# Kernel optimization log

Measured on AMD Instinct MI355X. Metric: run time of the kernel, lower is better.

Reference implementation:

```python
import jax, jax.numpy as jnp
import numpy as np

N_NODES = 100000
N_EDGES = 1600000
IN_DIM = 128
OUT_DIM = 128


def setup_inputs() -> dict:
    key = jax.random.key(0)
    k1, k2, k3, k4 = jax.random.split(key, 4)
    x = jax.random.normal(k1, (N_NODES, IN_DIM), dtype=jnp.float32)
    edge_index = jax.random.randint(k2, (2, N_EDGES), 0, N_NODES, dtype=jnp.int64)
    # glorot-ish linear weight, bias, and PReLU per-channel slope (torch default 0.25)
    W = jax.random.normal(k3, (IN_DIM, OUT_DIM), dtype=jnp.float32) * (1.0 / np.sqrt(IN_DIM))
    b = jax.random.normal(k4, (OUT_DIM,), dtype=jnp.float32) * 0.01
    alpha = jnp.full((OUT_DIM,), 0.25, dtype=jnp.float32)
    return {"x": x, "edge_index": edge_index, "W": W, "b": b, "alpha": alpha}


def reference(x, edge_index, W, b, alpha):
    N = x.shape[0]
    # add self loops (GCNConv default add_self_loops=True)
    loop = jnp.arange(N, dtype=edge_index.dtype)
    src = jnp.concatenate([edge_index[0], loop])  # [E+N]
    dst = jnp.concatenate([edge_index[1], loop])
    # symmetric normalization: deg computed at targets (includes self loops)
    ones = jnp.ones(dst.shape[0], dtype=x.dtype)
    deg = jax.ops.segment_sum(ones, dst, num_segments=N)  # [N]
    dinv = jnp.where(deg > 0, jax.lax.rsqrt(deg), 0.0)
    norm = dinv[src] * dinv[dst]  # [E+N]
    # dense linear transform, then gather-normalize-scatter aggregation
    h = x @ W  # [N, OUT_DIM]
    msg = h[src] * norm[:, None]  # [E+N, OUT_DIM]
    agg = jax.ops.segment_sum(msg, dst, num_segments=N) + b  # [N, OUT_DIM]
    # PReLU with per-channel slope
    z = jnp.where(agg > 0, agg, alpha * agg)
    return z
```

## Files before the change

kernel.cpp:

```cpp
#include <hip/hip_runtime.h>
#include <hip/hip_bf16.h>
#include <cstdint>

#define DIM 128
#define BK_SHIFT 7
#define BK_NODES 128
#define MAX_BUCKETS 1024
#define CUR_STRIDE 16
#define ST 4096
#define EPT 16
#define CAP 2560

typedef float f32x4  __attribute__((ext_vector_type(4)));
typedef short bf16x8 __attribute__((ext_vector_type(8)));

__device__ __forceinline__ unsigned bf16_rne(float f) {
    unsigned u = __float_as_uint(f);
    return (u + 0x7fffu + ((u >> 16) & 1u)) >> 16;
}

__global__ __launch_bounds__(256) void init_kernel(const float* __restrict__ x,
                                                   ushort* __restrict__ y,
                                                   const float* __restrict__ W,
                                                   ushort* __restrict__ Wt,
                                                   int* __restrict__ bcursor,
                                                   int N, int pb, int wb, int nbk) {
    int b = blockIdx.x, tid = threadIdx.x;
    if (b < pb) {
        int t = b * 256 + tid;
        if (t < N * (DIM / 4)) {
            float4 v = ((const float4*)x)[t];
            uint2 o;
            o.x = bf16_rne(v.x) | (bf16_rne(v.y) << 16);
            o.y = bf16_rne(v.z) | (bf16_rne(v.w) << 16);
            ((uint2*)y)[t] = o;
        }
    } else if (b < pb + wb) {
        int idx = (b - pb) * 256 + tid;
        if (idx < DIM * DIM) {
            int k = idx >> 7, c = idx & (DIM - 1);
            Wt[c * DIM + k] = (ushort)bf16_rne(W[idx]);
        }
    } else {
        int idx = (b - pb - wb) * 256 + tid;
        if (idx < nbk * CUR_STRIDE) bcursor[idx] = 0;
    }
}

__global__ __launch_bounds__(256) void scatter_kernel(const int* __restrict__ src,
                                                      const int* __restrict__ dst,
                                                      int* __restrict__ bcursor,
                                                      int* __restrict__ bbuf,
                                                      int E, int nbk) {
    __shared__ int h[MAX_BUCKETS];
    for (int i = threadIdx.x; i < nbk; i += 256) h[i] = 0;
    __syncthreads();
    int base = blockIdx.x * ST;
    int bk[EPT], rk[EPT], pk[EPT];
    #pragma unroll
    for (int k = 0; k < EPT; ++k) {
        int e = base + k * 256 + threadIdx.x;
        bk[k] = -1;
        if (e < E) {
            int d = dst[e];
            int b = ((unsigned)d) >> BK_SHIFT;
            bk[k] = b;
            pk[k] = (src[e] << BK_SHIFT) | (d & (BK_NODES - 1));
            rk[k] = atomicAdd(&h[b], 1);
        }
    }
    __syncthreads();
    for (int i = threadIdx.x; i < nbk; i += 256) {
        int c = h[i];
        h[i] = c ? atomicAdd(&bcursor[i * CUR_STRIDE], c) : 0;
    }
    __syncthreads();
    #pragma unroll
    for (int k = 0; k < EPT; ++k) {
        if (bk[k] >= 0) {
            int pos = h[bk[k]] + rk[k];
            if (pos < CAP) bbuf[(size_t)bk[k] * CAP + pos] = pk[k];
        }
    }
}

__global__ __launch_bounds__(256) void build_csr_kernel(const int* __restrict__ bbuf,
                                                        const int* __restrict__ bcursor,
                                                        int* __restrict__ obeg,
                                                        int* __restrict__ oend,
                                                        float* __restrict__ dinv,
                                                        int* __restrict__ csr_src,
                                                        int N) {
    __shared__ int cnt[BK_NODES];
    __shared__ int sc[BK_NODES];
    __shared__ int cur[BK_NODES];
    int b = blockIdx.x, tid = threadIdx.x;
    int count = bcursor[b * CUR_STRIDE];
    if (count > CAP) count = CAP;
    int base = b * CAP;
    if (tid < BK_NODES) cnt[tid] = 0;
    __syncthreads();
    for (int j = tid; j < count; j += 256)
        atomicAdd(&cnt[bbuf[base + j] & (BK_NODES - 1)], 1);
    __syncthreads();
    if (tid < BK_NODES) sc[tid] = cnt[tid];
    __syncthreads();
    for (int d = 1; d < BK_NODES; d <<= 1) {
        int v = (tid >= d && tid < BK_NODES) ? sc[tid - d] : 0;
        __syncthreads();
        if (tid < BK_NODES) sc[tid] += v;
        __syncthreads();
    }
    if (tid < BK_NODES) {
        int node = b * BK_NODES + tid;
        int start = base + sc[tid] - cnt[tid];
        cur[tid] = start;
        if (node < N) {
            obeg[node] = start;
            oend[node] = start + cnt[tid];
            dinv[node] = rsqrtf((float)(cnt[tid] + 1));
        }
    }
    __syncthreads();
    for (int j = tid; j < count; j += 256) {
        int p = bbuf[base + j];
        int pos = atomicAdd(&cur[p & (BK_NODES - 1)], 1);
        csr_src[pos] = p >> BK_SHIFT;
    }
}

__device__ __forceinline__ void agg_accum(float* a, uint4 v, float wt) {
    a[0] += wt * __uint_as_float(v.x << 16);
    a[1] += wt * __uint_as_float(v.x & 0xffff0000u);
    a[2] += wt * __uint_as_float(v.y << 16);
    a[3] += wt * __uint_as_float(v.y & 0xffff0000u);
    a[4] += wt * __uint_as_float(v.z << 16);
    a[5] += wt * __uint_as_float(v.z & 0xffff0000u);
    a[6] += wt * __uint_as_float(v.w << 16);
    a[7] += wt * __uint_as_float(v.w & 0xffff0000u);
}

__global__ __launch_bounds__(256) void agg_kernel(const ushort* __restrict__ y,
                                                  const int* __restrict__ csr_src,
                                                  const int* __restrict__ obeg,
                                                  const int* __restrict__ oend,
                                                  const float* __restrict__ dinv,
                                                  ushort* __restrict__ h, int N) {
    int lane = threadIdx.x & 63;
    int wid  = __builtin_amdgcn_readfirstlane((int)(threadIdx.x >> 6));
    int node = blockIdx.x * 4 + wid;
    if (node >= N) return;
    int g = lane >> 4;
    int m = lane & 15;
    int beg = obeg[node];
    int cnt = oend[node] - beg;
    float di = dinv[node];
    float a[8];
    #pragma unroll
    for (int c = 0; c < 8; ++c) a[c] = 0.f;

    {
        uint4 v = ((const uint4*)(y + (size_t)node * DIM))[m];
        agg_accum(a, v, (g == 0) ? di : 0.f);
    }

    int t = g;
    int nit = (cnt + 7) >> 3;
    for (int it = 0; it < nit; ++it, t += 8) {
        int tB = t + 4;
        int iA = beg + (t  < cnt ? t  : cnt - 1);
        int iB = beg + (tB < cnt ? tB : cnt - 1);
        int sA = csr_src[iA];
        int sB = csr_src[iB];
        float wA = (t  < cnt) ? dinv[sA] : 0.f;
        float wB = (tB < cnt) ? dinv[sB] : 0.f;
        uint4 vA = ((const uint4*)(y + (size_t)sA * DIM))[m];
        uint4 vB = ((const uint4*)(y + (size_t)sB * DIM))[m];
        agg_accum(a, vA, wA);
        agg_accum(a, vB, wB);
    }

    #pragma unroll
    for (int c = 0; c < 8; ++c) {
        a[c] += __shfl_xor(a[c], 16);
        a[c] += __shfl_xor(a[c], 32);
    }

    if (g == 0) {
        uint4 o;
        o.x = bf16_rne(di * a[0]) | (bf16_rne(di * a[1]) << 16);
        o.y = bf16_rne(di * a[2]) | (bf16_rne(di * a[3]) << 16);
        o.z = bf16_rne(di * a[4]) | (bf16_rne(di * a[5]) << 16);
        o.w = bf16_rne(di * a[6]) | (bf16_rne(di * a[7]) << 16);
        ((uint4*)(h + (size_t)node * DIM))[m] = o;
    }
}

__global__ __launch_bounds__(256) void gemm_kernel(const ushort* __restrict__ h,
                                                   const ushort* __restrict__ Wt,
                                                   const float* __restrict__ bias,
                                                   const float* __restrict__ alpha,
                                                   float* __restrict__ out, int N) {
    int lane = threadIdx.x & 63;
    int wv   = threadIdx.x >> 6;
    int rowbase = (blockIdx.x * 4 + wv) * 16;
    int r = lane & 15, quad = lane >> 4;
    f32x4 acc[8];
    #pragma unroll
    for (int ct = 0; ct < 8; ++ct) acc[ct] = (f32x4){0.f, 0.f, 0.f, 0.f};
    int arow = rowbase + r;
    if (arow >= N) arow = N - 1;
    const ushort* ap = h + (size_t)arow * DIM + quad * 8;
    #pragma unroll
    for (int ks = 0; ks < 4; ++ks) {
        bf16x8 a = *(const bf16x8*)(ap + ks * 32);
        #pragma unroll
        for (int ct = 0; ct < 8; ++ct) {
            bf16x8 b = *(const bf16x8*)(Wt + (size_t)(ct * 16 + r) * DIM + ks * 32 + quad * 8);
            acc[ct] = __builtin_amdgcn_mfma_f32_16x16x32_bf16(a, b, acc[ct], 0, 0, 0);
        }
    }
    #pragma unroll
    for (int ct = 0; ct < 8; ++ct) {
        int col = ct * 16 + r;
        float bb = bias[col], al = alpha[col];
        #pragma unroll
        for (int reg = 0; reg < 4; ++reg) {
            int grow = rowbase + quad * 4 + reg;
            if (grow < N) {
                float vv = acc[ct][reg] + bb;
                vv = vv > 0.f ? vv : al * vv;
                out[(size_t)grow * DIM + col] = vv;
            }
        }
    }
}

extern "C" void kernel_launch(void* const* d_in, const int* in_sizes, int n_in,
                              void* d_out, int out_size, void* d_ws, size_t ws_size,
                              hipStream_t stream) {
    const float* x     = (const float*)d_in[0];
    const int*   ei    = (const int*)d_in[1];
    const float* W     = (const float*)d_in[2];
    const float* bias  = (const float*)d_in[3];
    const float* alpha = (const float*)d_in[4];
    float* out = (float*)d_out;

    int N = in_sizes[0] / DIM;
    int E = in_sizes[1] / 2;
    const int* src = ei;
    const int* dst = ei + E;
    int nbk = (N + BK_NODES - 1) >> BK_SHIFT;

    char* ws = (char*)d_ws;
    size_t off = 0;
    auto alloc = [&](size_t bytes) -> char* {
        char* p = ws + off;
        off += (bytes + 255) & ~(size_t)255;
        return p;
    };
    size_t h_bytes    = (size_t)N * DIM * 2;
    size_t bbuf_bytes = (size_t)nbk * CAP * 4;
    char*   hreg    = alloc(h_bytes > bbuf_bytes ? h_bytes : bbuf_bytes);
    ushort* h       = (ushort*)hreg;
    int*    bbuf    = (int*)hreg;
    int*    csr_src = (int*)alloc((size_t)nbk * CAP * 4);
    ushort* y       = (ushort*)alloc((size_t)N * DIM * 2);
    int*    bcursor = (int*)alloc((size_t)nbk * CUR_STRIDE * 4);
    int*    obeg    = (int*)alloc((size_t)N * 4);
    int*    oend    = (int*)alloc((size_t)N * 4);
    float*  dinv    = (float*)alloc((size_t)N * 4);
    ushort* Wt      = (ushort*)alloc((size_t)DIM * DIM * 2);

    int pb = (N * (DIM / 4) + 255) / 256;
    int wb = (DIM * DIM + 255) / 256;
    int zb = (nbk * CUR_STRIDE + 255) / 256;

    init_kernel<<<pb + wb + zb, 256, 0, stream>>>(x, y, W, Wt, bcursor, N, pb, wb, nbk);
    scatter_kernel<<<(E + ST - 1) / ST, 256, 0, stream>>>(src, dst, bcursor, bbuf, E, nbk);
    build_csr_kernel<<<nbk, 256, 0, stream>>>(bbuf, bcursor, obeg, oend, dinv, csr_src, N);
    agg_kernel<<<(N + 3) / 4, 256, 0, stream>>>(y, csr_src, obeg, oend, dinv, h, N);
    gemm_kernel<<<(N + 63) / 64, 256, 0, stream>>>(h, Wt, bias, alpha, out, N);
}
```

Measured before the change: 262.5 us.

## Fuse neighbor aggregation and bf16 MFMA GEMM into one kernel via LDS

Merges the aggregation and dense transform kernels. Each 1024-thread block aggregates 16 nodes into a shared-memory tile, then 8 waves each compute one 16-column MFMA tile and apply bias and PReLU. This removes the global round trip of the intermediate bf16 h buffer and one kernel launch. In exchange, the block barrier makes the GEMM wait for the slowest node in the block, half the waves sit idle during the GEMM, and W is reloaded from global memory by every block.

```diff
diff --git a/kernel.cpp b/kernel.cpp
--- a/kernel.cpp
+++ b/kernel.cpp
@@ -10,6 +10,7 @@
 #define ST 4096
 #define EPT 16
 #define CAP 2560
+#define WPB 16
 
 typedef float f32x4  __attribute__((ext_vector_type(4)));
 typedef short bf16x8 __attribute__((ext_vector_type(8)));
@@ -140,50 +141,59 @@
     a[7] += wt * __uint_as_float(v.w & 0xffff0000u);
 }
 
-__global__ __launch_bounds__(256) void agg_kernel(const ushort* __restrict__ y,
-                                                  const int* __restrict__ csr_src,
-                                                  const int* __restrict__ obeg,
-                                                  const int* __restrict__ oend,
-                                                  const float* __restrict__ dinv,
-                                                  ushort* __restrict__ h, int N) {
-    int lane = threadIdx.x & 63;
-    int wid  = __builtin_amdgcn_readfirstlane((int)(threadIdx.x >> 6));
-    int node = blockIdx.x * 4 + wid;
-    if (node >= N) return;
+__global__ __launch_bounds__(1024) void agg_gemm_kernel(const ushort* __restrict__ y,
+                                                        const int* __restrict__ csr_src,
+                                                        const int* __restrict__ obeg,
+                                                        const int* __restrict__ oend,
+                                                        const float* __restrict__ dinv,
+                                                        const ushort* __restrict__ Wt,
+                                                        const float* __restrict__ bias,
+                                                        const float* __restrict__ alpha,
+                                                        float* __restrict__ out, int N) {
+    __shared__ ushort hT[WPB][136];
+    int tid  = threadIdx.x;
+    int lane = tid & 63;
+    int wid  = __builtin_amdgcn_readfirstlane((int)(tid >> 6));
+    int node = blockIdx.x * WPB + wid;
     int g = lane >> 4;
     int m = lane & 15;
-    int beg = obeg[node];
-    int cnt = oend[node] - beg;
-    float di = dinv[node];
+
     float a[8];
     #pragma unroll
     for (int c = 0; c < 8; ++c) a[c] = 0.f;
-
-    {
-        uint4 v = ((const uint4*)(y + (size_t)node * DIM))[m];
-        agg_accum(a, v, (g == 0) ? di : 0.f);
-    }
-
-    int t = g;
-    int nit = (cnt + 7) >> 3;
-    for (int it = 0; it < nit; ++it, t += 8) {
-        int tB = t + 4;
-        int iA = beg + (t  < cnt ? t  : cnt - 1);
-        int iB = beg + (tB < cnt ? tB : cnt - 1);
-        int sA = csr_src[iA];
-        int sB = csr_src[iB];
-        float wA = (t  < cnt) ? dinv[sA] : 0.f;
-        float wB = (tB < cnt) ? dinv[sB] : 0.f;
-        uint4 vA = ((const uint4*)(y + (size_t)sA * DIM))[m];
-        uint4 vB = ((const uint4*)(y + (size_t)sB * DIM))[m];
-        agg_accum(a, vA, wA);
-        agg_accum(a, vB, wB);
-    }
-
-    #pragma unroll
-    for (int c = 0; c < 8; ++c) {
-        a[c] += __shfl_xor(a[c], 16);
-        a[c] += __shfl_xor(a[c], 32);
+    float di = 0.f;
+
+    if (node < N) {
+        int beg = obeg[node];
+        int cnt = oend[node] - beg;
+        di = dinv[node];
+
+        {
+            uint4 v = ((const uint4*)(y + (size_t)node * DIM))[m];
+            agg_accum(a, v, (g == 0) ? di : 0.f);
+        }
+
+        int t = g;
+        int nit = (cnt + 7) >> 3;
+        for (int it = 0; it < nit; ++it, t += 8) {
+            int tB = t + 4;
+            int iA = beg + (t  < cnt ? t  : cnt - 1);
+            int iB = beg + (tB < cnt ? tB : cnt - 1);
+            int sA = csr_src[iA];
+            int sB = csr_src[iB];
+            float wA = (t  < cnt) ? dinv[sA] : 0.f;
+            float wB = (tB < cnt) ? dinv[sB] : 0.f;
+            uint4 vA = ((const uint4*)(y + (size_t)sA * DIM))[m];
+            uint4 vB = ((const uint4*)(y + (size_t)sB * DIM))[m];
+            agg_accum(a, vA, wA);
+            agg_accum(a, vB, wB);
+        }
+
+        #pragma unroll
+        for (int c = 0; c < 8; ++c) {
+            a[c] += __shfl_xor(a[c], 16);
+            a[c] += __shfl_xor(a[c], 32);
+        }
     }
 
     if (g == 0) {
@@ -192,43 +202,28 @@
         o.y = bf16_rne(di * a[2]) | (bf16_rne(di * a[3]) << 16);
         o.z = bf16_rne(di * a[4]) | (bf16_rne(di * a[5]) << 16);
         o.w = bf16_rne(di * a[6]) | (bf16_rne(di * a[7]) << 16);
-        ((uint4*)(h + (size_t)node * DIM))[m] = o;
-    }
-}
-
-__global__ __launch_bounds__(256) void gemm_kernel(const ushort* __restrict__ h,
-                                                   const ushort* __restrict__ Wt,
-                                                   const float* __restrict__ bias,
-                                                   const float* __restrict__ alpha,
-                                                   float* __restrict__ out, int N) {
-    int lane = threadIdx.x & 63;
-    int wv   = threadIdx.x >> 6;
-    int rowbase = (blockIdx.x * 4 + wv) * 16;
-    int r = lane & 15, quad = lane >> 4;
-    f32x4 acc[8];
-    #pragma unroll
-    for (int ct = 0; ct < 8; ++ct) acc[ct] = (f32x4){0.f, 0.f, 0.f, 0.f};
-    int arow = rowbase + r;
-    if (arow >= N) arow = N - 1;
-    const ushort* ap = h + (size_t)arow * DIM + quad * 8;
-    #pragma unroll
-    for (int ks = 0; ks < 4; ++ks) {
-        bf16x8 a = *(const bf16x8*)(ap + ks * 32);
+        *(uint4*)(&hT[wid][m * 8]) = o;
+    }
+    __syncthreads();
+
+    if (wid < 8) {
+        int r = lane & 15, quad = lane >> 4;
+        int ct = wid;
+        f32x4 acc = (f32x4){0.f, 0.f, 0.f, 0.f};
         #pragma unroll
-        for (int ct = 0; ct < 8; ++ct) {
-            bf16x8 b = *(const bf16x8*)(Wt + (size_t)(ct * 16 + r) * DIM + ks * 32 + quad * 8);
-            acc[ct] = __builtin_amdgcn_mfma_f32_16x16x32_bf16(a, b, acc[ct], 0, 0, 0);
-        }
-    }
-    #pragma unroll
-    for (int ct = 0; ct < 8; ++ct) {
+        for (int ks = 0; ks < 4; ++ks) {
+            bf16x8 av = *(const bf16x8*)(&hT[r][ks * 32 + quad * 8]);
+            bf16x8 bv = *(const bf16x8*)(Wt + (size_t)(ct * 16 + r) * DIM + ks * 32 + quad * 8);
+            acc = __builtin_amdgcn_mfma_f32_16x16x32_bf16(av, bv, acc, 0, 0, 0);
+        }
         int col = ct * 16 + r;
         float bb = bias[col], al = alpha[col];
+        int rowbase = blockIdx.x * WPB;
         #pragma unroll
         for (int reg = 0; reg < 4; ++reg) {
             int grow = rowbase + quad * 4 + reg;
             if (grow < N) {
-                float vv = acc[ct][reg] + bb;
+                float vv = acc[reg] + bb;
                 vv = vv > 0.f ? vv : al * vv;
                 out[(size_t)grow * DIM + col] = vv;
             }
@@ -259,11 +254,7 @@
         off += (bytes + 255) & ~(size_t)255;
         return p;
     };
-    size_t h_bytes    = (size_t)N * DIM * 2;
-    size_t bbuf_bytes = (size_t)nbk * CAP * 4;
-    char*   hreg    = alloc(h_bytes > bbuf_bytes ? h_bytes : bbuf_bytes);
-    ushort* h       = (ushort*)hreg;
-    int*    bbuf    = (int*)hreg;
+    int*    bbuf    = (int*)alloc((size_t)nbk * CAP * 4);
     int*    csr_src = (int*)alloc((size_t)nbk * CAP * 4);
     ushort* y       = (ushort*)alloc((size_t)N * DIM * 2);
     int*    bcursor = (int*)alloc((size_t)nbk * CUR_STRIDE * 4);
@@ -279,6 +270,6 @@
     init_kernel<<<pb + wb + zb, 256, 0, stream>>>(x, y, W, Wt, bcursor, N, pb, wb, nbk);
     scatter_kernel<<<(E + ST - 1) / ST, 256, 0, stream>>>(src, dst, bcursor, bbuf, E, nbk);
     build_csr_kernel<<<nbk, 256, 0, stream>>>(bbuf, bcursor, obeg, oend, dinv, csr_src, N);
-    agg_kernel<<<(N + 3) / 4, 256, 0, stream>>>(y, csr_src, obeg, oend, dinv, h, N);
-    gemm_kernel<<<(N + 63) / 64, 256, 0, stream>>>(h, Wt, bias, alpha, out, N);
-}
+    agg_gemm_kernel<<<(N + WPB - 1) / WPB, 1024, 0, stream>>>(y, csr_src, obeg, oend, dinv,
+                                                              Wt, bias, alpha, out, N);
+}
```

New measurement: 248.4 us. 5.4% less time.
